# Performance work log

Hardware: AMD Instinct MI355X
Metric: run time of the kernel (lower is better)

Reference implementation:

```python
import jax, jax.numpy as jnp
import numpy as np

B, P, D, G, N_IMGS, TEMP = 16, 4096, 512, 64, 5000, 0.01


def bilinear_grid_sample(img, grid):
    """F.grid_sample(img, grid, mode='bilinear', padding_mode='zeros', align_corners=False).
    img: (B, C, H, W); grid: (B, Hg, Wg, 2) with grid[...,0]=x, grid[...,1]=y in [-1,1].
    Returns (B, C, Hg*Wg)."""
    b, c, h, w = img.shape
    gx = grid[..., 0].reshape(b, -1)  # (B, N)
    gy = grid[..., 1].reshape(b, -1)
    # align_corners=False mapping to pixel coords
    ix = ((gx + 1.0) * w - 1.0) * 0.5
    iy = ((gy + 1.0) * h - 1.0) * 0.5
    ix0 = jnp.floor(ix)
    iy0 = jnp.floor(iy)
    ix1 = ix0 + 1.0
    iy1 = iy0 + 1.0
    wx1 = ix - ix0
    wx0 = 1.0 - wx1
    wy1 = iy - iy0
    wy0 = 1.0 - wy1
    flat = img.reshape(b, c, h * w)

    def gather(xi, yi):
        valid = (xi >= 0) & (xi < w) & (yi >= 0) & (yi < h)
        idx = (jnp.clip(yi, 0, h - 1) * w + jnp.clip(xi, 0, w - 1)).astype(jnp.int32)
        vals = jnp.take_along_axis(flat, jnp.broadcast_to(idx[:, None, :], (b, c, idx.shape[-1])), axis=2)
        return vals * valid[:, None, :].astype(img.dtype)

    out = (gather(ix0, iy0) * (wx0 * wy0)[:, None, :]
           + gather(ix1, iy0) * (wx1 * wy0)[:, None, :]
           + gather(ix0, iy1) * (wx0 * wy1)[:, None, :]
           + gather(ix1, iy1) * (wx1 * wy1)[:, None, :])
    return out  # (B, C, N)


def setup_inputs() -> dict:
    key = jax.random.key(0)
    ks = jax.random.split(key, 12)
    sc = 1.0 / np.sqrt(D)
    return {
        "x": jax.random.normal(ks[0], (B, P, D), dtype=jnp.float32),
        "Wq": jax.random.normal(ks[1], (D, D), dtype=jnp.float32) * sc,
        "bq": jnp.zeros((D,), dtype=jnp.float32),
        "Wk": jax.random.normal(ks[2], (D, D), dtype=jnp.float32) * sc,
        "bk": jnp.zeros((D,), dtype=jnp.float32),
        "Wv": jax.random.normal(ks[3], (D, D), dtype=jnp.float32) * sc,
        "bv": jnp.zeros((D,), dtype=jnp.float32),
        "avgs": jnp.zeros((N_IMGS, 2, P), dtype=jnp.float32),
        "std_devs": jnp.ones((N_IMGS, 2, P), dtype=jnp.float32),
        "noise_x": jax.random.normal(ks[4], (B, 1, P), dtype=jnp.float32),
        "noise_y": jax.random.normal(ks[5], (B, 1, P), dtype=jnp.float32),
        "img_ids": jax.random.randint(ks[6], (B,), 0, N_IMGS),
        "mask": jnp.ones((B, P), dtype=bool),
    }


def reference(x, Wq, bq, Wk, bk, Wv, bv, avgs, std_devs, noise_x, noise_y, img_ids, mask):
    b, s, d = x.shape
    q = x @ Wq.T + bq
    k = x @ Wk.T + bk
    v = x @ Wv.T + bv
    a = avgs[img_ids]       # (B, 2, P)
    sd = std_devs[img_ids]  # (B, 2, P)
    sample_x = jnp.tanh((noise_x + a[:, 0:1, :]) * sd[:, 0:1, :])  # (B,1,P)
    sample_y = jnp.tanh((noise_y + a[:, 1:2, :]) * sd[:, 1:2, :])  # (B,1,P)
    grid = jnp.concatenate([sample_x, sample_y], axis=1).reshape(b, G, G, 2)
    k_img = jnp.transpose(k, (0, 2, 1)).reshape(b, d, G, G)
    v_img = jnp.transpose(v, (0, 2, 1)).reshape(b, d, G, G)
    sampled_k = jnp.transpose(bilinear_grid_sample(k_img, grid), (0, 2, 1))  # (B, P, D)
    sampled_v = jnp.transpose(bilinear_grid_sample(v_img, grid), (0, 2, 1))
    scores = jnp.sum(sampled_k * q, axis=-1)  # (B, P)
    attention = jax.nn.sigmoid(TEMP * scores)[..., None] * sampled_v  # (B, P, D)
    return attention
```

## Files before the change

### kernel.cpp

```cpp
#include <hip/hip_runtime.h>
#include <math.h>


typedef __attribute__((ext_vector_type(8))) short s16x8;
typedef __attribute__((ext_vector_type(4))) float f32x4;

__device__ __forceinline__ unsigned short f2bf(float f) {
    unsigned u = __float_as_uint(f);
    u += 0x7FFFu + ((u >> 16) & 1u);
    return (unsigned short)(u >> 16);
}

__device__ __forceinline__ void gload_lds16(const void* g, void* l) {
    __builtin_amdgcn_global_load_lds(
        (const __attribute__((address_space(1))) unsigned int*)g,
        (__attribute__((address_space(3))) unsigned int*)l, 16, 0, 0);
}

__global__ __launch_bounds__(256) void cvt_all(
    const float* __restrict__ x, const float* __restrict__ Wq,
    const float* __restrict__ Wk, const float* __restrict__ Wv,
    unsigned short* __restrict__ xbf, unsigned short* __restrict__ wbf)
{
    const int i = blockIdx.x * 256 + threadIdx.x;
    const float* src;
    unsigned short* dst;
    size_t off;
    if (i < 4194304) {
        src = x; dst = xbf; off = (size_t)i;
    } else {
        int t = i - 4194304;
        int w = t >> 15;
        off = (size_t)(t & 32767);
        src = (w == 0) ? Wq : (w == 1 ? Wk : Wv);
        dst = wbf + (size_t)w * 512 * 512;
    }
    const float4* s = (const float4*)src + 2 * off;
    float4 a = s[0], b = s[1];
    uint4 o;
    o.x = (unsigned)f2bf(a.x) | ((unsigned)f2bf(a.y) << 16);
    o.y = (unsigned)f2bf(a.z) | ((unsigned)f2bf(a.w) << 16);
    o.z = (unsigned)f2bf(b.x) | ((unsigned)f2bf(b.y) << 16);
    o.w = (unsigned)f2bf(b.z) | ((unsigned)f2bf(b.w) << 16);
    ((uint4*)dst)[off] = o;
}

template<int T, int NVM, bool STAGE>
__device__ __forceinline__ void tile_step(
    char* ldsc, const unsigned short* aP, const unsigned short* bP,
    int tid, int abase, int bbase, f32x4 (&acc)[8][4])
{
    asm volatile("s_waitcnt vmcnt(%0)" :: "i"(NVM) : "memory");
    __builtin_amdgcn_s_barrier();
    __builtin_amdgcn_sched_barrier(0);
    const char* lp = ldsc + (T & 3) * 32768;
    s16x8 bfr[4], afA[4], afB[4];
    #pragma unroll
    for (int j = 0; j < 4; ++j) bfr[j] = *(const s16x8*)(lp + bbase + j * 256);
    #pragma unroll
    for (int u = 0; u < 4; ++u) afA[u] = *(const s16x8*)(lp + abase + u * 256);
    #pragma unroll
    for (int u = 0; u < 4; ++u) afB[u] = *(const s16x8*)(lp + abase + 1024 + u * 256);
    if (STAGE) {
        const int bo = ((T + 3) & 3) * 32768;
        gload_lds16(aP + (T + 3) * 32,      ldsc + bo + tid * 16);
        gload_lds16(aP + (T + 3) * 32 + 16, ldsc + bo + 8192 + tid * 16);
    }
    __builtin_amdgcn_s_barrier();
    asm volatile("s_waitcnt lgkmcnt(0)");
    __builtin_amdgcn_sched_barrier(0);
    __builtin_amdgcn_s_setprio(1);
    #pragma unroll
    for (int u = 0; u < 4; ++u)
        #pragma unroll
        for (int j = 0; j < 4; ++j)
            acc[u][j] = __builtin_amdgcn_mfma_f32_16x16x32_bf16(
                bfr[j], afA[u], acc[u][j], 0, 0, 0);
    __builtin_amdgcn_s_setprio(0);
    __builtin_amdgcn_s_barrier();
    __builtin_amdgcn_sched_barrier(0);
    if (STAGE) {
        const int bo = ((T + 3) & 3) * 32768;
        gload_lds16(bP + (T + 3) * 32,      ldsc + bo + 16384 + tid * 16);
        gload_lds16(bP + (T + 3) * 32 + 16, ldsc + bo + 24576 + tid * 16);
    }
    __builtin_amdgcn_s_setprio(1);
    #pragma unroll
    for (int u = 0; u < 4; ++u)
        #pragma unroll
        for (int j = 0; j < 4; ++j)
            acc[4 + u][j] = __builtin_amdgcn_mfma_f32_16x16x32_bf16(
                bfr[j], afB[u], acc[4 + u][j], 0, 0, 0);
    __builtin_amdgcn_s_setprio(0);
}

__global__ __launch_bounds__(512, 1) void qkv_gemm(
    const unsigned short* __restrict__ xbf,
    const unsigned short* __restrict__ wbf,
    const float* __restrict__ bq, const float* __restrict__ bk,
    const float* __restrict__ bv,
    unsigned short* __restrict__ qbf,
    unsigned short* __restrict__ kvbf)
{
    __shared__ __align__(16) short lds[4][16384];

    const int tid  = threadIdx.x;
    const int lane = tid & 63, wid = tid >> 6;
    const int wr = wid >> 2, wc = wid & 3;

    const int bid = blockIdx.x;
    const int wgid = (bid & 7) * 192 + (bid >> 3);
    const int mt = wgid / 6, nt = wgid % 6;
    const int m0 = mt * 256, n0 = nt * 256;

    const int srow = tid & 255;
    const unsigned short* aP = xbf + (size_t)(m0 + srow) * 512 + (tid >> 8) * 8;
    const unsigned short* bP = wbf + (size_t)(n0 + srow) * 512 + (tid >> 8) * 8;
    char* ldsc = (char*)lds;

    f32x4 acc[8][4] = {};

    const int abase = (lane >> 4) * 4096 + (wr * 128 + (lane & 15)) * 16;
    const int bbase = 16384 + (lane >> 4) * 4096 + (wc * 64 + (lane & 15)) * 16;

    #pragma unroll
    for (int t = 0; t < 3; ++t) {
        const int bo = t * 32768;
        gload_lds16(aP + t * 32,      ldsc + bo + tid * 16);
        gload_lds16(aP + t * 32 + 16, ldsc + bo + 8192 + tid * 16);
        gload_lds16(bP + t * 32,      ldsc + bo + 16384 + tid * 16);
        gload_lds16(bP + t * 32 + 16, ldsc + bo + 24576 + tid * 16);
    }

    tile_step< 0, 8, true >(ldsc, aP, bP, tid, abase, bbase, acc);
    tile_step< 1, 8, true >(ldsc, aP, bP, tid, abase, bbase, acc);
    tile_step< 2, 8, true >(ldsc, aP, bP, tid, abase, bbase, acc);
    tile_step< 3, 8, true >(ldsc, aP, bP, tid, abase, bbase, acc);
    tile_step< 4, 8, true >(ldsc, aP, bP, tid, abase, bbase, acc);
    tile_step< 5, 8, true >(ldsc, aP, bP, tid, abase, bbase, acc);
    tile_step< 6, 8, true >(ldsc, aP, bP, tid, abase, bbase, acc);
    tile_step< 7, 8, true >(ldsc, aP, bP, tid, abase, bbase, acc);
    tile_step< 8, 8, true >(ldsc, aP, bP, tid, abase, bbase, acc);
    tile_step< 9, 8, true >(ldsc, aP, bP, tid, abase, bbase, acc);
    tile_step<10, 8, true >(ldsc, aP, bP, tid, abase, bbase, acc);
    tile_step<11, 8, true >(ldsc, aP, bP, tid, abase, bbase, acc);
    tile_step<12, 8, true >(ldsc, aP, bP, tid, abase, bbase, acc);
    tile_step<13, 8, false>(ldsc, aP, bP, tid, abase, bbase, acc);
    tile_step<14, 4, false>(ldsc, aP, bP, tid, abase, bbase, acc);
    tile_step<15, 0, false>(ldsc, aP, bP, tid, abase, bbase, acc);

    const int sel = nt >> 1;
    const float* bias = sel == 0 ? bq : (sel == 1 ? bk : bv);
    const int rowl = wr * 128 + (lane & 15);
    const int coll = wc * 64 + ((lane >> 4) << 2);
    const int colg = (n0 & 511) + coll;

    __syncthreads();
    #pragma unroll
    for (int j = 0; j < 4; ++j) {
        const float4 b4 = *(const float4*)&bias[colg + j * 16];
        #pragma unroll
        for (int i = 0; i < 8; ++i) {
            const int row = rowl + i * 16;
            const int cb  = (coll + j * 16) * 2;
            const int byt = row * 512 + (((cb & ~15) ^ ((row & 7) << 4)) | (cb & 15));
            uint2 o;
            o.x = (unsigned)f2bf(acc[i][j][0] + b4.x)
                | ((unsigned)f2bf(acc[i][j][1] + b4.y) << 16);
            o.y = (unsigned)f2bf(acc[i][j][2] + b4.z)
                | ((unsigned)f2bf(acc[i][j][3] + b4.w) << 16);
            *(uint2*)(ldsc + byt) = o;
        }
    }
    __syncthreads();
    {
        unsigned short* dst = (sel == 0) ? qbf : kvbf;
        const int voff = (sel == 2) ? 512 : 0;
        const int rr = tid >> 5;
        const int cc = tid & 31;
        #pragma unroll
        for (int s = 0; s < 16; ++s) {
            const int r = s * 16 + rr;
            const int byt = r * 512 + ((cc * 16) ^ ((r & 7) << 4));
            uint4 d = *(const uint4*)(ldsc + byt);
            *(uint4*)&dst[(size_t)(m0 + r) * 1024 + voff + (n0 & 511) + cc * 8] = d;
        }
    }
}

__global__ __launch_bounds__(256) void sample_attn(
    float* __restrict__ qo,
    const unsigned short* __restrict__ kvbf,
    const float* __restrict__ avgs,
    const float* __restrict__ stds,
    const float* __restrict__ nx,
    const float* __restrict__ ny,
    const int* __restrict__ img_ids)
{
    const int lane = threadIdx.x & 63;
    const int wid  = threadIdx.x >> 6;
    const int point = (blockIdx.x << 2) + wid;
    const int b = point >> 12;
    const int n = point & 4095;
    const int g1 = n >> 6, g2 = n & 63;
    const int f0 = g1 * 128 + g2 * 2;
    const int id = img_ids[b];

    float g[2];
    #pragma unroll
    for (int c = 0; c < 2; ++c) {
        int f = f0 + c;
        int ch = f >> 12;
        int p  = f & 4095;
        float noise = ch ? ny[(size_t)b * 4096 + p] : nx[(size_t)b * 4096 + p];
        size_t o = ((size_t)id * 2 + ch) * 4096 + p;
        g[c] = tanhf((noise + avgs[o]) * stds[o]);
    }

    float ix = (g[0] + 1.0f) * 32.0f - 0.5f;
    float iy = (g[1] + 1.0f) * 32.0f - 0.5f;
    float fx0 = floorf(ix), fy0 = floorf(iy);
    float wx1 = ix - fx0, wx0 = 1.0f - wx1;
    float wy1 = iy - fy0, wy0 = 1.0f - wy1;
    int x0 = (int)fx0, y0 = (int)fy0;
    int x1 = x0 + 1, y1 = y0 + 1;
    bool vx0 = (x0 >= 0) & (x0 < 64), vx1 = (x1 >= 0) & (x1 < 64);
    bool vy0 = (y0 >= 0) & (y0 < 64), vy1 = (y1 >= 0) & (y1 < 64);
    float w00 = (vx0 & vy0) ? wx0 * wy0 : 0.0f;
    float w10 = (vx1 & vy0) ? wx1 * wy0 : 0.0f;
    float w01 = (vx0 & vy1) ? wx0 * wy1 : 0.0f;
    float w11 = (vx1 & vy1) ? wx1 * wy1 : 0.0f;
    int cx0 = min(max(x0, 0), 63), cx1 = min(max(x1, 0), 63);
    int cy0 = min(max(y0, 0), 63), cy1 = min(max(y1, 0), 63);

    const size_t base = (size_t)b * 4096;
    const size_t r00 = (base + (size_t)(cy0 * 64 + cx0)) * 1024;
    const size_t r10 = (base + (size_t)(cy0 * 64 + cx1)) * 1024;
    const size_t r01 = (base + (size_t)(cy1 * 64 + cx0)) * 1024;
    const size_t r11 = (base + (size_t)(cy1 * 64 + cx1)) * 1024;

    const int c = lane * 8;

    const unsigned short* qrowb =
        (const unsigned short*)qo + ((size_t)(b * 4096 + n)) * 1024;
    uint4 qu = *(const uint4*)(qrowb + c);
    float qv[8];
    {
        const unsigned* qp = (const unsigned*)&qu;
        #pragma unroll
        for (int t = 0; t < 4; ++t) {
            qv[2 * t]     = __uint_as_float(qp[t] << 16);
            qv[2 * t + 1] = __uint_as_float(qp[t] & 0xFFFF0000u);
        }
    }

    float sk[8], sv[8];
    {
        uint4 u00k = *(const uint4*)(kvbf + r00 + c);
        uint4 u10k = *(const uint4*)(kvbf + r10 + c);
        uint4 u01k = *(const uint4*)(kvbf + r01 + c);
        uint4 u11k = *(const uint4*)(kvbf + r11 + c);
        uint4 u00v = *(const uint4*)(kvbf + r00 + 512 + c);
        uint4 u10v = *(const uint4*)(kvbf + r10 + 512 + c);
        uint4 u01v = *(const uint4*)(kvbf + r01 + 512 + c);
        uint4 u11v = *(const uint4*)(kvbf + r11 + 512 + c);
        const unsigned* p00k = (const unsigned*)&u00k;
        const unsigned* p10k = (const unsigned*)&u10k;
        const unsigned* p01k = (const unsigned*)&u01k;
        const unsigned* p11k = (const unsigned*)&u11k;
        const unsigned* p00v = (const unsigned*)&u00v;
        const unsigned* p10v = (const unsigned*)&u10v;
        const unsigned* p01v = (const unsigned*)&u01v;
        const unsigned* p11v = (const unsigned*)&u11v;
        #pragma unroll
        for (int t = 0; t < 4; ++t) {
            float a00 = __uint_as_float(p00k[t] << 16);
            float b00 = __uint_as_float(p00k[t] & 0xFFFF0000u);
            float a10 = __uint_as_float(p10k[t] << 16);
            float b10 = __uint_as_float(p10k[t] & 0xFFFF0000u);
            float a01 = __uint_as_float(p01k[t] << 16);
            float b01 = __uint_as_float(p01k[t] & 0xFFFF0000u);
            float a11 = __uint_as_float(p11k[t] << 16);
            float b11 = __uint_as_float(p11k[t] & 0xFFFF0000u);
            sk[2 * t]     = w00 * a00 + w10 * a10 + w01 * a01 + w11 * a11;
            sk[2 * t + 1] = w00 * b00 + w10 * b10 + w01 * b01 + w11 * b11;
            a00 = __uint_as_float(p00v[t] << 16);
            b00 = __uint_as_float(p00v[t] & 0xFFFF0000u);
            a10 = __uint_as_float(p10v[t] << 16);
            b10 = __uint_as_float(p10v[t] & 0xFFFF0000u);
            a01 = __uint_as_float(p01v[t] << 16);
            b01 = __uint_as_float(p01v[t] & 0xFFFF0000u);
            a11 = __uint_as_float(p11v[t] << 16);
            b11 = __uint_as_float(p11v[t] & 0xFFFF0000u);
            sv[2 * t]     = w00 * a00 + w10 * a10 + w01 * a01 + w11 * a11;
            sv[2 * t + 1] = w00 * b00 + w10 * b10 + w01 * b01 + w11 * b11;
        }
    }

    float score = 0.0f;
    #pragma unroll
    for (int t = 0; t < 8; ++t) score += qv[t] * sk[t];
    #pragma unroll
    for (int off = 32; off > 0; off >>= 1)
        score += __shfl_xor(score, off);

    const float sig = 1.0f / (1.0f + expf(-0.01f * score));
    float* orow = qo + ((size_t)(b * 4096 + n)) * 512;
    float4 oA, oB;
    oA.x = sig * sv[0]; oA.y = sig * sv[1]; oA.z = sig * sv[2]; oA.w = sig * sv[3];
    oB.x = sig * sv[4]; oB.y = sig * sv[5]; oB.z = sig * sv[6]; oB.w = sig * sv[7];
    *(float4*)(orow + c) = oA;
    *(float4*)(orow + c + 4) = oB;
}

extern "C" void kernel_launch(void* const* d_in, const int* in_sizes, int n_in,
                              void* d_out, int out_size, void* d_ws, size_t ws_size,
                              hipStream_t stream)
{
    const float* x    = (const float*)d_in[0];
    const float* Wq   = (const float*)d_in[1];
    const float* bq   = (const float*)d_in[2];
    const float* Wk   = (const float*)d_in[3];
    const float* bk   = (const float*)d_in[4];
    const float* Wv   = (const float*)d_in[5];
    const float* bv   = (const float*)d_in[6];
    const float* avgs = (const float*)d_in[7];
    const float* stds = (const float*)d_in[8];
    const float* nx   = (const float*)d_in[9];
    const float* ny   = (const float*)d_in[10];
    const int* img_ids = (const int*)d_in[11];

    float* out = (float*)d_out;

    unsigned short* xbf  = (unsigned short*)d_ws;
    unsigned short* wbf  = xbf + (size_t)65536 * 512;
    unsigned short* kvbf = wbf + (size_t)1536 * 512;

    cvt_all<<<16768, 256, 0, stream>>>(x, Wq, Wk, Wv, xbf, wbf);

    qkv_gemm<<<1536, 512, 0, stream>>>(xbf, wbf, bq, bk, bv,
                                       (unsigned short*)d_out, kvbf);

    sample_attn<<<16384, 256, 0, stream>>>(out, kvbf, avgs, stds, nx, ny, img_ids);
}
```

Measured before the change: 294.6 us.

## Fuse fp32-to-bf16 conversion of x into the QKV GEMM tile loads

Drops the separate pass that converts x from fp32 to bf16. The GEMM now streams fp32 x tiles straight into LDS and converts them to bf16 in registers before the MFMAs, so only the weights keep a small conversion kernel. This saves a full write and re-read of a bf16 copy of x. In exchange the A tile takes twice the LDS and global traffic per step, the pipeline drops from four to three stages, and each step gains an extra barrier and conversion ALU work.

```diff
diff --git a/kernel.cpp b/kernel.cpp
--- a/kernel.cpp
+++ b/kernel.cpp
@@ -1,4 +1,5 @@
 #include <hip/hip_runtime.h>
+#include <hip/hip_bf16.h>
 #include <math.h>
 
 
@@ -11,30 +12,31 @@
     return (unsigned short)(u >> 16);
 }
 
+__device__ __forceinline__ s16x8 cvt8(f32x4 lo, f32x4 hi) {
+    s16x8 r;
+    #pragma unroll
+    for (int i = 0; i < 4; ++i) {
+        r[i]     = (short)__bfloat16_as_ushort(__float2bfloat16(lo[i]));
+        r[4 + i] = (short)__bfloat16_as_ushort(__float2bfloat16(hi[i]));
+    }
+    return r;
+}
+
 __device__ __forceinline__ void gload_lds16(const void* g, void* l) {
     __builtin_amdgcn_global_load_lds(
         (const __attribute__((address_space(1))) unsigned int*)g,
         (__attribute__((address_space(3))) unsigned int*)l, 16, 0, 0);
 }
 
-__global__ __launch_bounds__(256) void cvt_all(
-    const float* __restrict__ x, const float* __restrict__ Wq,
-    const float* __restrict__ Wk, const float* __restrict__ Wv,
-    unsigned short* __restrict__ xbf, unsigned short* __restrict__ wbf)
-{
-    const int i = blockIdx.x * 256 + threadIdx.x;
-    const float* src;
-    unsigned short* dst;
-    size_t off;
-    if (i < 4194304) {
-        src = x; dst = xbf; off = (size_t)i;
-    } else {
-        int t = i - 4194304;
-        int w = t >> 15;
-        off = (size_t)(t & 32767);
-        src = (w == 0) ? Wq : (w == 1 ? Wk : Wv);
-        dst = wbf + (size_t)w * 512 * 512;
-    }
+__global__ __launch_bounds__(256) void cvt_w(
+    const float* __restrict__ Wq, const float* __restrict__ Wk,
+    const float* __restrict__ Wv, unsigned short* __restrict__ wbf)
+{
+    const int t = blockIdx.x * 256 + threadIdx.x;
+    const int w = t >> 15;
+    const size_t off = (size_t)(t & 32767);
+    const float* src = (w == 0) ? Wq : (w == 1 ? Wk : Wv);
+    unsigned short* dst = wbf + (size_t)w * 512 * 512;
     const float4* s = (const float4*)src + 2 * off;
     float4 a = s[0], b = s[1];
     uint4 o;
@@ -47,62 +49,88 @@
 
 template<int T, int NVM, bool STAGE>
 __device__ __forceinline__ void tile_step(
-    char* ldsc, const unsigned short* aP, const unsigned short* bP,
+    char* ldsc, const float* aP, const unsigned short* bP,
     int tid, int abase, int bbase, f32x4 (&acc)[8][4])
 {
     asm volatile("s_waitcnt vmcnt(%0)" :: "i"(NVM) : "memory");
     __builtin_amdgcn_s_barrier();
     __builtin_amdgcn_sched_barrier(0);
-    const char* lp = ldsc + (T & 3) * 32768;
-    s16x8 bfr[4], afA[4], afB[4];
+    const char* lp = ldsc + (T % 3) * 49152;
+    s16x8 bfr[4];
+    f32x4 alo[4], ahi[4];
     #pragma unroll
     for (int j = 0; j < 4; ++j) bfr[j] = *(const s16x8*)(lp + bbase + j * 256);
     #pragma unroll
-    for (int u = 0; u < 4; ++u) afA[u] = *(const s16x8*)(lp + abase + u * 256);
-    #pragma unroll
-    for (int u = 0; u < 4; ++u) afB[u] = *(const s16x8*)(lp + abase + 1024 + u * 256);
+    for (int u = 0; u < 4; ++u) {
+        alo[u] = *(const f32x4*)(lp + abase + u * 256);
+        ahi[u] = *(const f32x4*)(lp + abase + u * 256 + 4096);
+    }
     if (STAGE) {
-        const int bo = ((T + 3) & 3) * 32768;
-        gload_lds16(aP + (T + 3) * 32,      ldsc + bo + tid * 16);
-        gload_lds16(aP + (T + 3) * 32 + 16, ldsc + bo + 8192 + tid * 16);
+        const int so = ((T + 2) % 3) * 49152;
+        const int kb = (T + 2) * 32 + (tid >> 8) * 4;
+        const int db = so + (tid >> 8) * 4096 + (tid & 255) * 16;
+        gload_lds16(aP + kb,      ldsc + db);
+        gload_lds16(aP + kb + 8,  ldsc + db + 8192);
+        gload_lds16(aP + kb + 16, ldsc + db + 16384);
+        gload_lds16(aP + kb + 24, ldsc + db + 24576);
     }
     __builtin_amdgcn_s_barrier();
     asm volatile("s_waitcnt lgkmcnt(0)");
     __builtin_amdgcn_sched_barrier(0);
-    __builtin_amdgcn_s_setprio(1);
-    #pragma unroll
-    for (int u = 0; u < 4; ++u)
-        #pragma unroll
-        for (int j = 0; j < 4; ++j)
-            acc[u][j] = __builtin_amdgcn_mfma_f32_16x16x32_bf16(
-                bfr[j], afA[u], acc[u][j], 0, 0, 0);
-    __builtin_amdgcn_s_setprio(0);
+    {
+        s16x8 af[4];
+        #pragma unroll
+        for (int u = 0; u < 4; ++u) af[u] = cvt8(alo[u], ahi[u]);
+        __builtin_amdgcn_s_setprio(1);
+        #pragma unroll
+        for (int u = 0; u < 4; ++u)
+            #pragma unroll
+            for (int j = 0; j < 4; ++j)
+                acc[u][j] = __builtin_amdgcn_mfma_f32_16x16x32_bf16(
+                    bfr[j], af[u], acc[u][j], 0, 0, 0);
+        __builtin_amdgcn_s_setprio(0);
+    }
     __builtin_amdgcn_s_barrier();
     __builtin_amdgcn_sched_barrier(0);
+    #pragma unroll
+    for (int u = 0; u < 4; ++u) {
+        alo[u] = *(const f32x4*)(lp + abase + 1024 + u * 256);
+        ahi[u] = *(const f32x4*)(lp + abase + 1024 + u * 256 + 4096);
+    }
     if (STAGE) {
-        const int bo = ((T + 3) & 3) * 32768;
-        gload_lds16(bP + (T + 3) * 32,      ldsc + bo + 16384 + tid * 16);
-        gload_lds16(bP + (T + 3) * 32 + 16, ldsc + bo + 24576 + tid * 16);
-    }
-    __builtin_amdgcn_s_setprio(1);
-    #pragma unroll
-    for (int u = 0; u < 4; ++u)
-        #pragma unroll
-        for (int j = 0; j < 4; ++j)
-            acc[4 + u][j] = __builtin_amdgcn_mfma_f32_16x16x32_bf16(
-                bfr[j], afB[u], acc[4 + u][j], 0, 0, 0);
-    __builtin_amdgcn_s_setprio(0);
+        const int so = ((T + 2) % 3) * 49152;
+        const int kb = (T + 2) * 32 + (tid >> 8) * 8;
+        const int db = so + 32768 + (tid >> 8) * 4096 + (tid & 255) * 16;
+        gload_lds16(bP + kb,      ldsc + db);
+        gload_lds16(bP + kb + 16, ldsc + db + 8192);
+    }
+    __builtin_amdgcn_s_barrier();
+    asm volatile("s_waitcnt lgkmcnt(0)");
+    __builtin_amdgcn_sched_barrier(0);
+    {
+        s16x8 af[4];
+        #pragma unroll
+        for (int u = 0; u < 4; ++u) af[u] = cvt8(alo[u], ahi[u]);
+        __builtin_amdgcn_s_setprio(1);
+        #pragma unroll
+        for (int u = 0; u < 4; ++u)
+            #pragma unroll
+            for (int j = 0; j < 4; ++j)
+                acc[4 + u][j] = __builtin_amdgcn_mfma_f32_16x16x32_bf16(
+                    bfr[j], af[u], acc[4 + u][j], 0, 0, 0);
+        __builtin_amdgcn_s_setprio(0);
+    }
 }
 
 __global__ __launch_bounds__(512, 1) void qkv_gemm(
-    const unsigned short* __restrict__ xbf,
+    const float* __restrict__ x,
     const unsigned short* __restrict__ wbf,
     const float* __restrict__ bq, const float* __restrict__ bk,
     const float* __restrict__ bv,
     unsigned short* __restrict__ qbf,
     unsigned short* __restrict__ kvbf)
 {
-    __shared__ __align__(16) short lds[4][16384];
+    __shared__ __align__(16) char lds[3][49152];
 
     const int tid  = threadIdx.x;
     const int lane = tid & 63, wid = tid >> 6;
@@ -114,39 +142,45 @@
     const int m0 = mt * 256, n0 = nt * 256;
 
     const int srow = tid & 255;
-    const unsigned short* aP = xbf + (size_t)(m0 + srow) * 512 + (tid >> 8) * 8;
-    const unsigned short* bP = wbf + (size_t)(n0 + srow) * 512 + (tid >> 8) * 8;
+    const float* aP = x + (size_t)(m0 + srow) * 512;
+    const unsigned short* bP = wbf + (size_t)(n0 + srow) * 512;
     char* ldsc = (char*)lds;
 
     f32x4 acc[8][4] = {};
 
-    const int abase = (lane >> 4) * 4096 + (wr * 128 + (lane & 15)) * 16;
-    const int bbase = 16384 + (lane >> 4) * 4096 + (wc * 64 + (lane & 15)) * 16;
-
-    #pragma unroll
-    for (int t = 0; t < 3; ++t) {
-        const int bo = t * 32768;
-        gload_lds16(aP + t * 32,      ldsc + bo + tid * 16);
-        gload_lds16(aP + t * 32 + 16, ldsc + bo + 8192 + tid * 16);
-        gload_lds16(bP + t * 32,      ldsc + bo + 16384 + tid * 16);
-        gload_lds16(bP + t * 32 + 16, ldsc + bo + 24576 + tid * 16);
-    }
-
-    tile_step< 0, 8, true >(ldsc, aP, bP, tid, abase, bbase, acc);
-    tile_step< 1, 8, true >(ldsc, aP, bP, tid, abase, bbase, acc);
-    tile_step< 2, 8, true >(ldsc, aP, bP, tid, abase, bbase, acc);
-    tile_step< 3, 8, true >(ldsc, aP, bP, tid, abase, bbase, acc);
-    tile_step< 4, 8, true >(ldsc, aP, bP, tid, abase, bbase, acc);
-    tile_step< 5, 8, true >(ldsc, aP, bP, tid, abase, bbase, acc);
-    tile_step< 6, 8, true >(ldsc, aP, bP, tid, abase, bbase, acc);
-    tile_step< 7, 8, true >(ldsc, aP, bP, tid, abase, bbase, acc);
-    tile_step< 8, 8, true >(ldsc, aP, bP, tid, abase, bbase, acc);
-    tile_step< 9, 8, true >(ldsc, aP, bP, tid, abase, bbase, acc);
-    tile_step<10, 8, true >(ldsc, aP, bP, tid, abase, bbase, acc);
-    tile_step<11, 8, true >(ldsc, aP, bP, tid, abase, bbase, acc);
-    tile_step<12, 8, true >(ldsc, aP, bP, tid, abase, bbase, acc);
-    tile_step<13, 8, false>(ldsc, aP, bP, tid, abase, bbase, acc);
-    tile_step<14, 4, false>(ldsc, aP, bP, tid, abase, bbase, acc);
+    const int abase = (lane >> 4) * 8192 + (wr * 128 + (lane & 15)) * 16;
+    const int bbase = 32768 + (lane >> 4) * 4096 + (wc * 64 + (lane & 15)) * 16;
+
+    #pragma unroll
+    for (int t = 0; t < 2; ++t) {
+        const int so = t * 49152;
+        const int ka = t * 32 + (tid >> 8) * 4;
+        const int da = so + (tid >> 8) * 4096 + (tid & 255) * 16;
+        gload_lds16(aP + ka,      ldsc + da);
+        gload_lds16(aP + ka + 8,  ldsc + da + 8192);
+        gload_lds16(aP + ka + 16, ldsc + da + 16384);
+        gload_lds16(aP + ka + 24, ldsc + da + 24576);
+        const int kb = t * 32 + (tid >> 8) * 8;
+        const int db = so + 32768 + (tid >> 8) * 4096 + (tid & 255) * 16;
+        gload_lds16(bP + kb,      ldsc + db);
+        gload_lds16(bP + kb + 16, ldsc + db + 8192);
+    }
+
+    tile_step< 0, 6, true >(ldsc, aP, bP, tid, abase, bbase, acc);
+    tile_step< 1, 6, true >(ldsc, aP, bP, tid, abase, bbase, acc);
+    tile_step< 2, 6, true >(ldsc, aP, bP, tid, abase, bbase, acc);
+    tile_step< 3, 6, true >(ldsc, aP, bP, tid, abase, bbase, acc);
+    tile_step< 4, 6, true >(ldsc, aP, bP, tid, abase, bbase, acc);
+    tile_step< 5, 6, true >(ldsc, aP, bP, tid, abase, bbase, acc);
+    tile_step< 6, 6, true >(ldsc, aP, bP, tid, abase, bbase, acc);
+    tile_step< 7, 6, true >(ldsc, aP, bP, tid, abase, bbase, acc);
+    tile_step< 8, 6, true >(ldsc, aP, bP, tid, abase, bbase, acc);
+    tile_step< 9, 6, true >(ldsc, aP, bP, tid, abase, bbase, acc);
+    tile_step<10, 6, true >(ldsc, aP, bP, tid, abase, bbase, acc);
+    tile_step<11, 6, true >(ldsc, aP, bP, tid, abase, bbase, acc);
+    tile_step<12, 6, true >(ldsc, aP, bP, tid, abase, bbase, acc);
+    tile_step<13, 6, true >(ldsc, aP, bP, tid, abase, bbase, acc);
+    tile_step<14, 6, false>(ldsc, aP, bP, tid, abase, bbase, acc);
     tile_step<15, 0, false>(ldsc, aP, bP, tid, abase, bbase, acc);
 
     const int sel = nt >> 1;
@@ -332,13 +366,12 @@
 
     float* out = (float*)d_out;
 
-    unsigned short* xbf  = (unsigned short*)d_ws;
-    unsigned short* wbf  = xbf + (size_t)65536 * 512;
+    unsigned short* wbf  = (unsigned short*)d_ws;
     unsigned short* kvbf = wbf + (size_t)1536 * 512;
 
-    cvt_all<<<16768, 256, 0, stream>>>(x, Wq, Wk, Wv, xbf, wbf);
-
-    qkv_gemm<<<1536, 512, 0, stream>>>(xbf, wbf, bq, bk, bv,
+    cvt_w<<<384, 256, 0, stream>>>(Wq, Wk, Wv, wbf);
+
+    qkv_gemm<<<1536, 512, 0, stream>>>(x, wbf, bq, bk, bv,
                                        (unsigned short*)d_out, kvbf);
 
     sample_attn<<<16384, 256, 0, stream>>>(out, kvbf, avgs, stds, nx, ny, img_ids);
```

Result: slower. 322.8 us (+9.6%).

## Make QKV GEMM persistent over N tiles, prefetching next tile during epilogue

Applied to the files above, without the earlier changes.

The QKV GEMM now launches 256 workgroups, one per 256-row M tile, and each loops over all six N tiles instead of launching 1536 independent workgroups. The first K stages of the next N tile are issued before the epilogue, and the epilogue is split into four 64-row chunks staged through the fourth LDS buffer, so global loads overlap bias-add and store. This is meant to hide pipeline fill and drain per tile and improve reuse of the A rows. In exchange it cuts the workgroup count to 256, roughly one per CU, and adds barriers in the chunked epilogue.

```diff
diff --git a/kernel.cpp b/kernel.cpp
--- a/kernel.cpp
+++ b/kernel.cpp
@@ -94,6 +94,17 @@
     __builtin_amdgcn_s_setprio(0);
 }
 
+__device__ __forceinline__ void stage_tile(
+    char* ldsc, const unsigned short* aP, const unsigned short* bP,
+    int tid, int kt, int buf)
+{
+    const int bo = buf * 32768;
+    gload_lds16(aP + kt * 32,      ldsc + bo + tid * 16);
+    gload_lds16(aP + kt * 32 + 16, ldsc + bo + 8192 + tid * 16);
+    gload_lds16(bP + kt * 32,      ldsc + bo + 16384 + tid * 16);
+    gload_lds16(bP + kt * 32 + 16, ldsc + bo + 24576 + tid * 16);
+}
+
 __global__ __launch_bounds__(512, 1) void qkv_gemm(
     const unsigned short* __restrict__ xbf,
     const unsigned short* __restrict__ wbf,
@@ -102,89 +113,109 @@
     unsigned short* __restrict__ qbf,
     unsigned short* __restrict__ kvbf)
 {
-    __shared__ __align__(16) short lds[4][16384];
+    __shared__ __align__(16) char lds[4][32768];
 
     const int tid  = threadIdx.x;
     const int lane = tid & 63, wid = tid >> 6;
     const int wr = wid >> 2, wc = wid & 3;
 
     const int bid = blockIdx.x;
-    const int wgid = (bid & 7) * 192 + (bid >> 3);
-    const int mt = wgid / 6, nt = wgid % 6;
-    const int m0 = mt * 256, n0 = nt * 256;
+    const int mt = (bid & 7) * 32 + (bid >> 3);
+    const int m0 = mt * 256;
 
     const int srow = tid & 255;
     const unsigned short* aP = xbf + (size_t)(m0 + srow) * 512 + (tid >> 8) * 8;
-    const unsigned short* bP = wbf + (size_t)(n0 + srow) * 512 + (tid >> 8) * 8;
     char* ldsc = (char*)lds;
-
-    f32x4 acc[8][4] = {};
 
     const int abase = (lane >> 4) * 4096 + (wr * 128 + (lane & 15)) * 16;
     const int bbase = 16384 + (lane >> 4) * 4096 + (wc * 64 + (lane & 15)) * 16;
 
-    #pragma unroll
-    for (int t = 0; t < 3; ++t) {
-        const int bo = t * 32768;
-        gload_lds16(aP + t * 32,      ldsc + bo + tid * 16);
-        gload_lds16(aP + t * 32 + 16, ldsc + bo + 8192 + tid * 16);
-        gload_lds16(bP + t * 32,      ldsc + bo + 16384 + tid * 16);
-        gload_lds16(bP + t * 32 + 16, ldsc + bo + 24576 + tid * 16);
-    }
-
-    tile_step< 0, 8, true >(ldsc, aP, bP, tid, abase, bbase, acc);
-    tile_step< 1, 8, true >(ldsc, aP, bP, tid, abase, bbase, acc);
-    tile_step< 2, 8, true >(ldsc, aP, bP, tid, abase, bbase, acc);
-    tile_step< 3, 8, true >(ldsc, aP, bP, tid, abase, bbase, acc);
-    tile_step< 4, 8, true >(ldsc, aP, bP, tid, abase, bbase, acc);
-    tile_step< 5, 8, true >(ldsc, aP, bP, tid, abase, bbase, acc);
-    tile_step< 6, 8, true >(ldsc, aP, bP, tid, abase, bbase, acc);
-    tile_step< 7, 8, true >(ldsc, aP, bP, tid, abase, bbase, acc);
-    tile_step< 8, 8, true >(ldsc, aP, bP, tid, abase, bbase, acc);
-    tile_step< 9, 8, true >(ldsc, aP, bP, tid, abase, bbase, acc);
-    tile_step<10, 8, true >(ldsc, aP, bP, tid, abase, bbase, acc);
-    tile_step<11, 8, true >(ldsc, aP, bP, tid, abase, bbase, acc);
-    tile_step<12, 8, true >(ldsc, aP, bP, tid, abase, bbase, acc);
-    tile_step<13, 8, false>(ldsc, aP, bP, tid, abase, bbase, acc);
-    tile_step<14, 4, false>(ldsc, aP, bP, tid, abase, bbase, acc);
-    tile_step<15, 0, false>(ldsc, aP, bP, tid, abase, bbase, acc);
-
-    const int sel = nt >> 1;
-    const float* bias = sel == 0 ? bq : (sel == 1 ? bk : bv);
     const int rowl = wr * 128 + (lane & 15);
     const int coll = wc * 64 + ((lane >> 4) << 2);
-    const int colg = (n0 & 511) + coll;
-
-    __syncthreads();
-    #pragma unroll
-    for (int j = 0; j < 4; ++j) {
-        const float4 b4 = *(const float4*)&bias[colg + j * 16];
-        #pragma unroll
-        for (int i = 0; i < 8; ++i) {
-            const int row = rowl + i * 16;
-            const int cb  = (coll + j * 16) * 2;
-            const int byt = row * 512 + (((cb & ~15) ^ ((row & 7) << 4)) | (cb & 15));
-            uint2 o;
-            o.x = (unsigned)f2bf(acc[i][j][0] + b4.x)
-                | ((unsigned)f2bf(acc[i][j][1] + b4.y) << 16);
-            o.y = (unsigned)f2bf(acc[i][j][2] + b4.z)
-                | ((unsigned)f2bf(acc[i][j][3] + b4.w) << 16);
-            *(uint2*)(ldsc + byt) = o;
+
+    {
+        const unsigned short* bP0 = wbf + (size_t)srow * 512 + (tid >> 8) * 8;
+        stage_tile(ldsc, aP, bP0, tid, 0, 0);
+        stage_tile(ldsc, aP, bP0, tid, 1, 1);
+        stage_tile(ldsc, aP, bP0, tid, 2, 2);
+    }
+
+    for (int nt = 0; nt < 6; ++nt) {
+        const int n0 = nt * 256;
+        const unsigned short* bP = wbf + (size_t)(n0 + srow) * 512 + (tid >> 8) * 8;
+        const unsigned short* bPn = bP + (size_t)256 * 512;
+
+        f32x4 acc[8][4] = {};
+
+        tile_step< 0, 8, true >(ldsc, aP, bP, tid, abase, bbase, acc);
+        tile_step< 1, 8, true >(ldsc, aP, bP, tid, abase, bbase, acc);
+        tile_step< 2, 8, true >(ldsc, aP, bP, tid, abase, bbase, acc);
+        tile_step< 3, 8, true >(ldsc, aP, bP, tid, abase, bbase, acc);
+        tile_step< 4, 8, true >(ldsc, aP, bP, tid, abase, bbase, acc);
+        tile_step< 5, 8, true >(ldsc, aP, bP, tid, abase, bbase, acc);
+        tile_step< 6, 8, true >(ldsc, aP, bP, tid, abase, bbase, acc);
+        tile_step< 7, 8, true >(ldsc, aP, bP, tid, abase, bbase, acc);
+        tile_step< 8, 8, true >(ldsc, aP, bP, tid, abase, bbase, acc);
+        tile_step< 9, 8, true >(ldsc, aP, bP, tid, abase, bbase, acc);
+        tile_step<10, 8, true >(ldsc, aP, bP, tid, abase, bbase, acc);
+        tile_step<11, 8, true >(ldsc, aP, bP, tid, abase, bbase, acc);
+        tile_step<12, 8, true >(ldsc, aP, bP, tid, abase, bbase, acc);
+        tile_step<13, 8, false>(ldsc, aP, bP, tid, abase, bbase, acc);
+        tile_step<14, 4, false>(ldsc, aP, bP, tid, abase, bbase, acc);
+        tile_step<15, 0, false>(ldsc, aP, bP, tid, abase, bbase, acc);
+
+        if (nt < 5) {
+            stage_tile(ldsc, aP, bPn, tid, 0, 0);
+            stage_tile(ldsc, aP, bPn, tid, 1, 1);
         }
-    }
-    __syncthreads();
-    {
+
+        const int sel = nt >> 1;
+        const float* bias = sel == 0 ? bq : (sel == 1 ? bk : bv);
+        const int colg = (nt & 1) * 256 + coll;
         unsigned short* dst = (sel == 0) ? qbf : kvbf;
         const int voff = (sel == 2) ? 512 : 0;
-        const int rr = tid >> 5;
-        const int cc = tid & 31;
-        #pragma unroll
-        for (int s = 0; s < 16; ++s) {
-            const int r = s * 16 + rr;
-            const int byt = r * 512 + ((cc * 16) ^ ((r & 7) << 4));
-            uint4 d = *(const uint4*)(ldsc + byt);
-            *(uint4*)&dst[(size_t)(m0 + r) * 1024 + voff + (n0 & 511) + cc * 8] = d;
+
+        __syncthreads();
+        #pragma unroll
+        for (int ch = 0; ch < 4; ++ch) {
+            if (wr == (ch >> 1)) {
+                #pragma unroll
+                for (int j = 0; j < 4; ++j) {
+                    const float4 b4 = *(const float4*)&bias[colg + j * 16];
+                    #pragma unroll
+                    for (int ii = 0; ii < 4; ++ii) {
+                        const int i = (ch & 1) * 4 + ii;
+                        const int lr = (rowl + i * 16) & 63;
+                        const int cb = (coll + j * 16) * 2;
+                        const int byt = 3 * 32768 + lr * 512 +
+                            (((cb & ~15) ^ ((lr & 7) << 4)) | (cb & 15));
+                        uint2 o;
+                        o.x = (unsigned)f2bf(acc[i][j][0] + b4.x)
+                            | ((unsigned)f2bf(acc[i][j][1] + b4.y) << 16);
+                        o.y = (unsigned)f2bf(acc[i][j][2] + b4.z)
+                            | ((unsigned)f2bf(acc[i][j][3] + b4.w) << 16);
+                        *(uint2*)(ldsc + byt) = o;
+                    }
+                }
+            }
+            __syncthreads();
+            {
+                const int lr = tid >> 3;
+                const int co = (tid & 7) * 64;
+                #pragma unroll
+                for (int q = 0; q < 4; ++q) {
+                    const int cbyte = co + q * 16;
+                    const int byt = 3 * 32768 + lr * 512 +
+                                    (cbyte ^ ((lr & 7) << 4));
+                    uint4 d = *(const uint4*)(ldsc + byt);
+                    *(uint4*)&dst[(size_t)(m0 + ch * 64 + lr) * 1024 + voff
+                                  + (nt & 1) * 256 + cbyte / 2] = d;
+                }
+            }
+            __syncthreads();
         }
+
+        if (nt < 5) stage_tile(ldsc, aP, bPn, tid, 2, 2);
     }
 }
 
@@ -338,8 +369,8 @@
 
     cvt_all<<<16768, 256, 0, stream>>>(x, Wq, Wk, Wv, xbf, wbf);
 
-    qkv_gemm<<<1536, 512, 0, stream>>>(xbf, wbf, bq, bk, bv,
-                                       (unsigned short*)d_out, kvbf);
+    qkv_gemm<<<256, 512, 0, stream>>>(xbf, wbf, bq, bk, bv,
+                                      (unsigned short*)d_out, kvbf);
 
     sample_attn<<<16384, 256, 0, stream>>>(out, kvbf, avgs, stds, nx, ny, img_ids);
 }
```

After: 413.8 us. 40.5% more time.
